# Kernel tuning notes

Hardware: AMD Instinct MI355X
Metric: run time of the kernel (lower is better)

The kernel has to match this reference:

```python
import jax, jax.numpy as jnp
import numpy as np

N, DEG, IN_DIM, HID, OUT = 50000, 32, 256, 256, 128

def setup_inputs() -> dict:
    key = jax.random.key(0)
    k1, k2, k3, k4, k5, k6 = jax.random.split(key, 6)
    node_features = jax.random.normal(k1, (N, IN_DIM), dtype=jnp.float32)
    neighbor_idx = jax.random.randint(k2, (N, DEG), 0, N)
    scale1 = 1.0 / np.sqrt(2 * IN_DIM)
    scale2 = 1.0 / np.sqrt(HID)
    W1 = jax.random.normal(k3, (HID, 2 * IN_DIM), dtype=jnp.float32) * scale1
    b1 = jax.random.normal(k4, (HID,), dtype=jnp.float32) * scale1
    W2 = jax.random.normal(k5, (OUT, HID), dtype=jnp.float32) * scale2
    b2 = jax.random.normal(k6, (OUT,), dtype=jnp.float32) * scale2
    return {"node_features": node_features, "neighbor_idx": neighbor_idx,
            "W1": W1, "b1": b1, "W2": W2, "b2": b2}

def reference(node_features, neighbor_idx, W1, b1, W2, b2):
    # Layer 0 (mean aggregator, with neighbors):
    # gather [N, DEG, IN_DIM] neighbor features, mean over DEG
    nbr_mean = jnp.mean(node_features[neighbor_idx], axis=1)  # [N, IN_DIM]
    combined = jnp.concatenate([node_features, nbr_mean], axis=-1)  # [N, 2*IN_DIM]
    h = jax.nn.relu(combined @ W1.T + b1)  # [N, HID]
    # Layer 1: empty neighbor list -> linear_without_neighbors + relu
    out = jax.nn.relu(h @ W2.T + b2)  # [N, OUT]
    return out
```

## Files before the change

### kernel.cpp

```cpp
#include <hip/hip_runtime.h>
#include <stdint.h>

#define N_NODES 50000
#define DEG     32
#define IN_DIM  256
#define K1      512
#define HID     256
#define OUT_DIM 128

#define NCHUNK  4
#define CDIM    64
#define SLICE8  ((size_t)N_NODES * CDIM)
#define GT      16

#define MT     32
#define NTILES ((N_NODES + MT - 1) / MT)
#define GBLK   512
#define CSTR   520
#define HSTR   264

typedef __bf16 bf16x8 __attribute__((ext_vector_type(8)));
typedef float  f32x4  __attribute__((ext_vector_type(4)));
typedef float  f32x2  __attribute__((ext_vector_type(2)));

#define PIN(x) asm volatile("" : "+v"(x))

__device__ __forceinline__ unsigned short f2bf(float f) {
    union { float f; unsigned u; } v; v.f = f;
    unsigned r = v.u + 0x7fffu + ((v.u >> 16) & 1u);
    return (unsigned short)(r >> 16);
}
__device__ __forceinline__ int clampN(int v) {
    return v < 0 ? 0 : (v >= N_NODES ? N_NODES - 1 : v);
}
__device__ __forceinline__ void async_copy16(const void* g, void* l) {
    __builtin_amdgcn_global_load_lds(
        (const __attribute__((address_space(1))) void*)g,
        (__attribute__((address_space(3))) void*)l, 16, 0, 0);
}

#define FEAT_BLKS ((N_NODES + 7) / 8)
__global__ __launch_bounds__(256)
void prep_all(const float* __restrict__ feat,
              const float* __restrict__ W1, const float* __restrict__ W2,
              const int*   __restrict__ nbr,
              unsigned short* __restrict__ featb,
              unsigned char*  __restrict__ featF8,
              unsigned short* __restrict__ W1b, unsigned short* __restrict__ W2b,
              unsigned short* __restrict__ nbr16)
{
    const int t = threadIdx.x;
    if (blockIdx.x < FEAT_BLKS) {
        const int node = blockIdx.x * 8 + (t >> 5);
        const int seg  = t & 31;
        if (node < N_NODES) {
            const float4* src = (const float4*)(feat + (size_t)node * IN_DIM + seg * 8);
            float4 f0 = src[0], f1 = src[1];
            ushort4 o0, o1;
            o0.x = f2bf(f0.x); o0.y = f2bf(f0.y); o0.z = f2bf(f0.z); o0.w = f2bf(f0.w);
            o1.x = f2bf(f1.x); o1.y = f2bf(f1.y); o1.z = f2bf(f1.z); o1.w = f2bf(f1.w);
            unsigned short* db = featb + (size_t)node * IN_DIM + seg * 8;
            *(ushort4*)db       = o0;
            *(ushort4*)(db + 4) = o1;
            int u0 = 0, u1 = 0;
            u0 = __builtin_amdgcn_cvt_pk_fp8_f32(f0.x, f0.y, u0, false);
            u0 = __builtin_amdgcn_cvt_pk_fp8_f32(f0.z, f0.w, u0, true);
            u1 = __builtin_amdgcn_cvt_pk_fp8_f32(f1.x, f1.y, u1, false);
            u1 = __builtin_amdgcn_cvt_pk_fp8_f32(f1.z, f1.w, u1, true);
            const int c   = seg >> 3;
            const int off = (seg & 7) * 8;
            unsigned char* d8 = featF8 + (size_t)c * SLICE8 + (size_t)node * CDIM + off;
            ((int*)d8)[0] = u0;
            ((int*)d8)[1] = u1;
        }
    } else {
        const int bid = blockIdx.x - FEAT_BLKS;
        const int stride = 256 * 256 * 4;
        const int tid4 = (bid * 256 + t) * 4;
        for (int i = tid4; i < HID * K1; i += stride) {
            float4 f = *(const float4*)(W1 + i);
            ushort4 o; o.x = f2bf(f.x); o.y = f2bf(f.y); o.z = f2bf(f.z); o.w = f2bf(f.w);
            *(ushort4*)(W1b + i) = o;
        }
        for (int i = tid4; i < OUT_DIM * HID; i += stride) {
            float4 f = *(const float4*)(W2 + i);
            ushort4 o; o.x = f2bf(f.x); o.y = f2bf(f.y); o.z = f2bf(f.z); o.w = f2bf(f.w);
            *(ushort4*)(W2b + i) = o;
        }
        for (int i = tid4; i < N_NODES * DEG; i += stride) {
            int4 v = *(const int4*)(nbr + i);
            ushort4 o;
            o.x = (unsigned short)clampN(v.x); o.y = (unsigned short)clampN(v.y);
            o.z = (unsigned short)clampN(v.z); o.w = (unsigned short)clampN(v.w);
            *(ushort4*)(nbr16 + i) = o;
        }
    }
}

__global__ __launch_bounds__(256)
void gather_mean_fp8(const unsigned char*  __restrict__ featF8,
                     const unsigned short* __restrict__ nbr16,
                     unsigned short*       __restrict__ meanb)
{
    __shared__ unsigned short sIdx[GT * DEG];
    const int tid  = threadIdx.x;
    const int c    = blockIdx.y;
    const int base = blockIdx.x * GT;

    if (tid < 128) {
        *(ushort4*)(sIdx + tid * 4) =
            *(const ushort4*)(nbr16 + (size_t)base * DEG + tid * 4);
    }
    __syncthreads();

    const unsigned char* slice = featF8 + (size_t)c * SLICE8;
    const int grp = tid >> 4;
    const int ln  = tid & 15;
    const unsigned short* idxr = sIdx + grp * DEG;

    unsigned vv[DEG];
    #pragma unroll
    for (int j = 0; j < DEG; ++j) {
        int nb = idxr[j];
        vv[j] = *(const unsigned*)(slice + (size_t)nb * CDIM + ln * 4);
    }
    float s0 = 0.f, s1 = 0.f, s2 = 0.f, s3 = 0.f;
    #pragma unroll
    for (int j = 0; j < DEG; ++j) {
        f32x2 lo = __builtin_amdgcn_cvt_pk_f32_fp8(vv[j], false);
        f32x2 hi = __builtin_amdgcn_cvt_pk_f32_fp8(vv[j], true);
        s0 += lo[0]; s1 += lo[1]; s2 += hi[0]; s3 += hi[1];
    }
    const float sc = 1.0f / 32.0f;
    ushort4 o;
    o.x = f2bf(s0 * sc); o.y = f2bf(s1 * sc);
    o.z = f2bf(s2 * sc); o.w = f2bf(s3 * sc);
    const int node = base + grp;
    *(ushort4*)(meanb + (size_t)node * IN_DIM + c * CDIM + ln * 4) = o;
}

__global__ __launch_bounds__(512, 2)
void sage_gemm(const unsigned short* __restrict__ featb,
               const unsigned short* __restrict__ meanb,
               const unsigned short* __restrict__ W1b,
               const float*          __restrict__ b1,
               const unsigned short* __restrict__ W2b,
               const float*          __restrict__ b2,
               float*                __restrict__ out)
{
    __shared__ __align__(16) unsigned short sC[MT * CSTR];
    __shared__ __align__(16) unsigned short sH[MT * HSTR];

    const int tid  = threadIdx.x;
    const int lane = tid & 63;
    const int wave = tid >> 6;
    const int r    = lane & 15;
    const int q    = lane >> 4;

    bf16x8 w1f[2][16];
    #pragma unroll
    for (int nt = 0; nt < 2; ++nt) {
        const size_t nrow = (size_t)(wave * 32 + nt * 16 + r) * K1;
        #pragma unroll
        for (int kk = 0; kk < 16; ++kk) {
            w1f[nt][kk] = *(const bf16x8*)(W1b + nrow + kk * 32 + q * 8);
            PIN(w1f[nt][kk]);
        }
    }
    bf16x8 w2f[8];
    {
        const size_t orow = (size_t)(wave * 16 + r) * HID;
        #pragma unroll
        for (int kk = 0; kk < 8; ++kk) {
            w2f[kk] = *(const bf16x8*)(W2b + orow + kk * 32 + q * 8);
            PIN(w2f[kk]);
        }
    }
    const float bias1a = b1[wave * 32 + r];
    const float bias1b = b1[wave * 32 + 16 + r];
    const float bias2  = b2[wave * 16 + r];

    auto stage = [&](int tile) {
        const int base = tile * MT;
        #pragma unroll
        for (int j = 0; j < 4; ++j) {
            const int i = wave * 4 + j;
            int node = base + i;
            if (node >= N_NODES) node = N_NODES - 1;
            const unsigned short* g = (lane < 32)
                ? featb + (size_t)node * IN_DIM + lane * 8
                : meanb + (size_t)node * IN_DIM + (lane - 32) * 8;
            async_copy16(g, &sC[i * CSTR]);
        }
    };

    int tile = blockIdx.x;
    if (tile < NTILES) stage(tile);

    for (; tile < NTILES; tile += GBLK) {
        __syncthreads();

        {
            f32x4 acc[2][2];
            #pragma unroll
            for (int mt = 0; mt < 2; ++mt)
                #pragma unroll
                for (int nt = 0; nt < 2; ++nt)
                    acc[mt][nt] = (f32x4){0.f, 0.f, 0.f, 0.f};

            #pragma unroll
            for (int kk = 0; kk < 16; ++kk) {
                bf16x8 a0 = *(const bf16x8*)(&sC[r * CSTR + kk * 32 + q * 8]);
                bf16x8 a1 = *(const bf16x8*)(&sC[(16 + r) * CSTR + kk * 32 + q * 8]);
                acc[0][0] = __builtin_amdgcn_mfma_f32_16x16x32_bf16(a0, w1f[0][kk], acc[0][0], 0, 0, 0);
                acc[1][0] = __builtin_amdgcn_mfma_f32_16x16x32_bf16(a1, w1f[0][kk], acc[1][0], 0, 0, 0);
                acc[0][1] = __builtin_amdgcn_mfma_f32_16x16x32_bf16(a0, w1f[1][kk], acc[0][1], 0, 0, 0);
                acc[1][1] = __builtin_amdgcn_mfma_f32_16x16x32_bf16(a1, w1f[1][kk], acc[1][1], 0, 0, 0);
            }
            #pragma unroll
            for (int nt = 0; nt < 2; ++nt) {
                const int n = wave * 32 + nt * 16 + r;
                const float bias = nt ? bias1b : bias1a;
                #pragma unroll
                for (int mt = 0; mt < 2; ++mt)
                    #pragma unroll
                    for (int g = 0; g < 4; ++g) {
                        const int m = mt * 16 + q * 4 + g;
                        float v = acc[mt][nt][g] + bias;
                        sH[m * HSTR + n] = f2bf(v > 0.f ? v : 0.f);
                    }
            }
        }
        __syncthreads();

        const int nxt = tile + GBLK;
        if (nxt < NTILES) stage(nxt);

        {
            f32x4 acc3[2];
            acc3[0] = (f32x4){0.f, 0.f, 0.f, 0.f};
            acc3[1] = (f32x4){0.f, 0.f, 0.f, 0.f};
            #pragma unroll
            for (int kk = 0; kk < 8; ++kk) {
                bf16x8 h0 = *(const bf16x8*)(&sH[r * HSTR + kk * 32 + q * 8]);
                bf16x8 h1 = *(const bf16x8*)(&sH[(16 + r) * HSTR + kk * 32 + q * 8]);
                acc3[0] = __builtin_amdgcn_mfma_f32_16x16x32_bf16(h0, w2f[kk], acc3[0], 0, 0, 0);
                acc3[1] = __builtin_amdgcn_mfma_f32_16x16x32_bf16(h1, w2f[kk], acc3[1], 0, 0, 0);
            }
            const int base = tile * MT;
            const int o = wave * 16 + r;
            #pragma unroll
            for (int mt = 0; mt < 2; ++mt)
                #pragma unroll
                for (int g = 0; g < 4; ++g) {
                    const int m = mt * 16 + q * 4 + g;
                    const int node = base + m;
                    if (node < N_NODES) {
                        float v = acc3[mt][g] + bias2;
                        out[(size_t)node * OUT_DIM + o] = v > 0.f ? v : 0.f;
                    }
                }
        }
    }
}

__global__ __launch_bounds__(256)
void sage_naive(const float* __restrict__ feat, const int* __restrict__ nbr,
                const float* __restrict__ W1, const float* __restrict__ b1,
                const float* __restrict__ W2, const float* __restrict__ b2,
                float* __restrict__ out) {
    __shared__ float comb[K1];
    __shared__ float h[HID];
    const int node = blockIdx.x;
    const int t = threadIdx.x;
    comb[t] = feat[(size_t)node * IN_DIM + t];
    float acc = 0.f;
    for (int d = 0; d < DEG; ++d) {
        int nb = clampN(nbr[node * DEG + d]);
        acc += feat[(size_t)nb * IN_DIM + t];
    }
    comb[IN_DIM + t] = acc * (1.0f / 32.0f);
    __syncthreads();
    float s = b1[t];
    for (int k = 0; k < K1; ++k) s += comb[k] * W1[(size_t)t * K1 + k];
    h[t] = s > 0.f ? s : 0.f;
    __syncthreads();
    if (t < OUT_DIM) {
        float s2 = b2[t];
        for (int k = 0; k < HID; ++k) s2 += h[k] * W2[(size_t)t * HID + k];
        out[(size_t)node * OUT_DIM + t] = s2 > 0.f ? s2 : 0.f;
    }
}

extern "C" void kernel_launch(void* const* d_in, const int* in_sizes, int n_in,
                              void* d_out, int out_size, void* d_ws, size_t ws_size,
                              hipStream_t stream) {
    const float* feat = (const float*)d_in[0];
    const int*   nbr  = (const int*)d_in[1];
    const float* W1   = (const float*)d_in[2];
    const float* b1   = (const float*)d_in[3];
    const float* W2   = (const float*)d_in[4];
    const float* b2   = (const float*)d_in[5];
    float* out = (float*)d_out;

    const size_t feat_elems = (size_t)N_NODES * IN_DIM;
    const size_t w1_elems   = (size_t)HID * K1;
    const size_t w2_elems   = (size_t)OUT_DIM * HID;
    const size_t mean_elems = (size_t)N_NODES * IN_DIM;
    const size_t idx_elems  = (size_t)N_NODES * DEG;
    const size_t u16_elems  = feat_elems + w1_elems + w2_elems + mean_elems + idx_elems;
    const size_t need = u16_elems * sizeof(unsigned short)
                      + (size_t)NCHUNK * SLICE8;

    if (ws_size >= need) {
        unsigned short* featb  = (unsigned short*)d_ws;
        unsigned short* W1b    = featb + feat_elems;
        unsigned short* W2b    = W1b + w1_elems;
        unsigned short* meanb  = W2b + w2_elems;
        unsigned short* nbr16  = meanb + mean_elems;
        unsigned char*  featF8 = (unsigned char*)(nbr16 + idx_elems);

        prep_all<<<FEAT_BLKS + 256, 256, 0, stream>>>(feat, W1, W2, nbr,
                                                      featb, featF8, W1b, W2b, nbr16);
        gather_mean_fp8<<<dim3(N_NODES / GT, NCHUNK), 256, 0, stream>>>(featF8, nbr16, meanb);
        sage_gemm<<<GBLK, 512, 0, stream>>>(featb, meanb, W1b, b1, W2b, b2, out);
    } else {
        sage_naive<<<N_NODES, 256, 0, stream>>>(feat, nbr, W1, b1, W2, b2, out);
    }
}
```

Baseline: 181.2 us.

## Replace persistent register-resident-weight GEMM with LDS-staged K-chunked tiled GEMM

```diff
diff --git a/kernel.cpp b/kernel.cpp
--- a/kernel.cpp
+++ b/kernel.cpp
@@ -13,17 +13,14 @@
 #define SLICE8  ((size_t)N_NODES * CDIM)
 #define GT      16
 
-#define MT     32
-#define NTILES ((N_NODES + MT - 1) / MT)
-#define GBLK   512
-#define CSTR   520
-#define HSTR   264
+#define MT2    64
+#define NT2B   ((N_NODES + MT2 - 1) / MT2)
+#define KC     64
+#define HSTR2  264
 
 typedef __bf16 bf16x8 __attribute__((ext_vector_type(8)));
 typedef float  f32x4  __attribute__((ext_vector_type(4)));
 typedef float  f32x2  __attribute__((ext_vector_type(2)));
-
-#define PIN(x) asm volatile("" : "+v"(x))
 
 __device__ __forceinline__ unsigned short f2bf(float f) {
     union { float f; unsigned u; } v; v.f = f;
@@ -140,127 +137,142 @@
 }
 
 __global__ __launch_bounds__(512, 2)
-void sage_gemm(const unsigned short* __restrict__ featb,
-               const unsigned short* __restrict__ meanb,
-               const unsigned short* __restrict__ W1b,
-               const float*          __restrict__ b1,
-               const unsigned short* __restrict__ W2b,
-               const float*          __restrict__ b2,
-               float*                __restrict__ out)
+void sage_gemm2(const unsigned short* __restrict__ featb,
+                const unsigned short* __restrict__ meanb,
+                const unsigned short* __restrict__ W1b,
+                const float*          __restrict__ b1,
+                const unsigned short* __restrict__ W2b,
+                const float*          __restrict__ b2,
+                float*                __restrict__ out)
 {
-    __shared__ __align__(16) unsigned short sC[MT * CSTR];
-    __shared__ __align__(16) unsigned short sH[MT * HSTR];
+    __shared__ __align__(16) unsigned short sA[MT2 * KC];
+    __shared__ __align__(16) unsigned short sW[256 * KC];
+    __shared__ __align__(16) unsigned short sH[MT2 * HSTR2];
 
     const int tid  = threadIdx.x;
     const int lane = tid & 63;
     const int wave = tid >> 6;
     const int r    = lane & 15;
     const int q    = lane >> 4;
-
-    bf16x8 w1f[2][16];
-    #pragma unroll
-    for (int nt = 0; nt < 2; ++nt) {
-        const size_t nrow = (size_t)(wave * 32 + nt * 16 + r) * K1;
-        #pragma unroll
-        for (int kk = 0; kk < 16; ++kk) {
-            w1f[nt][kk] = *(const bf16x8*)(W1b + nrow + kk * 32 + q * 8);
-            PIN(w1f[nt][kk]);
-        }
-    }
-    bf16x8 w2f[8];
-    {
-        const size_t orow = (size_t)(wave * 16 + r) * HID;
-        #pragma unroll
-        for (int kk = 0; kk < 8; ++kk) {
-            w2f[kk] = *(const bf16x8*)(W2b + orow + kk * 32 + q * 8);
-            PIN(w2f[kk]);
-        }
-    }
-    const float bias1a = b1[wave * 32 + r];
-    const float bias1b = b1[wave * 32 + 16 + r];
-    const float bias2  = b2[wave * 16 + r];
-
-    auto stage = [&](int tile) {
-        const int base = tile * MT;
+    const int mh   = wave >> 2;
+    const int nq   = wave & 3;
+
+    const int tbase = blockIdx.x * MT2;
+
+    f32x4 acc1[2][4];
+    #pragma unroll
+    for (int mt = 0; mt < 2; ++mt)
+        #pragma unroll
+        for (int nt = 0; nt < 4; ++nt)
+            acc1[mt][nt] = (f32x4){0.f, 0.f, 0.f, 0.f};
+
+    for (int kc = 0; kc < 8; ++kc) {
+        __syncthreads();
+        {
+            const int i = wave * 8 + (lane >> 3);
+            const int node = clampN(tbase + i);
+            const int g = (lane & 7) ^ (i & 7);
+            const unsigned short* src = (kc < 4 ? featb : meanb)
+                + (size_t)node * IN_DIM + (kc & 3) * KC + g * 8;
+            async_copy16(src, &sA[wave * 8 * KC]);
+        }
         #pragma unroll
         for (int j = 0; j < 4; ++j) {
-            const int i = wave * 4 + j;
-            int node = base + i;
-            if (node >= N_NODES) node = N_NODES - 1;
-            const unsigned short* g = (lane < 32)
-                ? featb + (size_t)node * IN_DIM + lane * 8
-                : meanb + (size_t)node * IN_DIM + (lane - 32) * 8;
-            async_copy16(g, &sC[i * CSTR]);
-        }
-    };
-
-    int tile = blockIdx.x;
-    if (tile < NTILES) stage(tile);
-
-    for (; tile < NTILES; tile += GBLK) {
+            const int n = wave * 32 + j * 8 + (lane >> 3);
+            const int g = (lane & 7) ^ (n & 7);
+            async_copy16(W1b + (size_t)n * K1 + kc * KC + g * 8,
+                         &sW[(wave * 32 + j * 8) * KC]);
+        }
         __syncthreads();
 
-        {
-            f32x4 acc[2][2];
+        #pragma unroll
+        for (int kk = 0; kk < 2; ++kk) {
+            bf16x8 a[2], w[4];
+            #pragma unroll
+            for (int mt = 0; mt < 2; ++mt)
+                a[mt] = *(const bf16x8*)(&sA[(mh * 32 + mt * 16 + r) * KC
+                                             + ((kk * 4 + q) ^ (r & 7)) * 8]);
+            #pragma unroll
+            for (int nt = 0; nt < 4; ++nt)
+                w[nt] = *(const bf16x8*)(&sW[(nq * 64 + nt * 16 + r) * KC
+                                             + ((kk * 4 + q) ^ (r & 7)) * 8]);
+            #pragma unroll
+            for (int mt = 0; mt < 2; ++mt)
+                #pragma unroll
+                for (int nt = 0; nt < 4; ++nt)
+                    acc1[mt][nt] = __builtin_amdgcn_mfma_f32_16x16x32_bf16(
+                        a[mt], w[nt], acc1[mt][nt], 0, 0, 0);
+        }
+    }
+
+    #pragma unroll
+    for (int nt = 0; nt < 4; ++nt) {
+        const int n = nq * 64 + nt * 16 + r;
+        const float bias = b1[n];
+        #pragma unroll
+        for (int mt = 0; mt < 2; ++mt)
+            #pragma unroll
+            for (int g = 0; g < 4; ++g) {
+                const int m = mh * 32 + mt * 16 + q * 4 + g;
+                float v = acc1[mt][nt][g] + bias;
+                sH[m * HSTR2 + n] = f2bf(v > 0.f ? v : 0.f);
+            }
+    }
+
+    const int nh = wave & 3;
+    f32x4 acc2[2][2];
+    #pragma unroll
+    for (int mt = 0; mt < 2; ++mt)
+        #pragma unroll
+        for (int nt = 0; nt < 2; ++nt)
+            acc2[mt][nt] = (f32x4){0.f, 0.f, 0.f, 0.f};
+
+    for (int kc = 0; kc < 4; ++kc) {
+        __syncthreads();
+        #pragma unroll
+        for (int j = 0; j < 2; ++j) {
+            const int n = wave * 16 + j * 8 + (lane >> 3);
+            const int g = (lane & 7) ^ (n & 7);
+            async_copy16(W2b + (size_t)n * HID + kc * KC + g * 8,
+                         &sW[(wave * 16 + j * 8) * KC]);
+        }
+        __syncthreads();
+
+        #pragma unroll
+        for (int kk = 0; kk < 2; ++kk) {
+            bf16x8 h[2], w[2];
+            #pragma unroll
+            for (int mt = 0; mt < 2; ++mt)
+                h[mt] = *(const bf16x8*)(&sH[(mh * 32 + mt * 16 + r) * HSTR2
+                                             + kc * KC + kk * 32 + q * 8]);
+            #pragma unroll
+            for (int nt = 0; nt < 2; ++nt)
+                w[nt] = *(const bf16x8*)(&sW[(nh * 32 + nt * 16 + r) * KC
+                                             + ((kk * 4 + q) ^ (r & 7)) * 8]);
             #pragma unroll
             for (int mt = 0; mt < 2; ++mt)
                 #pragma unroll
                 for (int nt = 0; nt < 2; ++nt)
-                    acc[mt][nt] = (f32x4){0.f, 0.f, 0.f, 0.f};
-
-            #pragma unroll
-            for (int kk = 0; kk < 16; ++kk) {
-                bf16x8 a0 = *(const bf16x8*)(&sC[r * CSTR + kk * 32 + q * 8]);
-                bf16x8 a1 = *(const bf16x8*)(&sC[(16 + r) * CSTR + kk * 32 + q * 8]);
-                acc[0][0] = __builtin_amdgcn_mfma_f32_16x16x32_bf16(a0, w1f[0][kk], acc[0][0], 0, 0, 0);
-                acc[1][0] = __builtin_amdgcn_mfma_f32_16x16x32_bf16(a1, w1f[0][kk], acc[1][0], 0, 0, 0);
-                acc[0][1] = __builtin_amdgcn_mfma_f32_16x16x32_bf16(a0, w1f[1][kk], acc[0][1], 0, 0, 0);
-                acc[1][1] = __builtin_amdgcn_mfma_f32_16x16x32_bf16(a1, w1f[1][kk], acc[1][1], 0, 0, 0);
+                    acc2[mt][nt] = __builtin_amdgcn_mfma_f32_16x16x32_bf16(
+                        h[mt], w[nt], acc2[mt][nt], 0, 0, 0);
+        }
+    }
+
+    #pragma unroll
+    for (int nt = 0; nt < 2; ++nt) {
+        const int o = nh * 32 + nt * 16 + r;
+        const float bias = b2[o];
+        #pragma unroll
+        for (int mt = 0; mt < 2; ++mt)
+            #pragma unroll
+            for (int g = 0; g < 4; ++g) {
+                const int m = mh * 32 + mt * 16 + q * 4 + g;
+                const int node = tbase + m;
+                if (node < N_NODES) {
+                    float v = acc2[mt][nt][g] + bias;
+                    out[(size_t)node * OUT_DIM + o] = v > 0.f ? v : 0.f;
+                }
             }
-            #pragma unroll
-            for (int nt = 0; nt < 2; ++nt) {
-                const int n = wave * 32 + nt * 16 + r;
-                const float bias = nt ? bias1b : bias1a;
-                #pragma unroll
-                for (int mt = 0; mt < 2; ++mt)
-                    #pragma unroll
-                    for (int g = 0; g < 4; ++g) {
-                        const int m = mt * 16 + q * 4 + g;
-                        float v = acc[mt][nt][g] + bias;
-                        sH[m * HSTR + n] = f2bf(v > 0.f ? v : 0.f);
-                    }
-            }
-        }
-        __syncthreads();
-
-        const int nxt = tile + GBLK;
-        if (nxt < NTILES) stage(nxt);
-
-        {
-            f32x4 acc3[2];
-            acc3[0] = (f32x4){0.f, 0.f, 0.f, 0.f};
-            acc3[1] = (f32x4){0.f, 0.f, 0.f, 0.f};
-            #pragma unroll
-            for (int kk = 0; kk < 8; ++kk) {
-                bf16x8 h0 = *(const bf16x8*)(&sH[r * HSTR + kk * 32 + q * 8]);
-                bf16x8 h1 = *(const bf16x8*)(&sH[(16 + r) * HSTR + kk * 32 + q * 8]);
-                acc3[0] = __builtin_amdgcn_mfma_f32_16x16x32_bf16(h0, w2f[kk], acc3[0], 0, 0, 0);
-                acc3[1] = __builtin_amdgcn_mfma_f32_16x16x32_bf16(h1, w2f[kk], acc3[1], 0, 0, 0);
-            }
-            const int base = tile * MT;
-            const int o = wave * 16 + r;
-            #pragma unroll
-            for (int mt = 0; mt < 2; ++mt)
-                #pragma unroll
-                for (int g = 0; g < 4; ++g) {
-                    const int m = mt * 16 + q * 4 + g;
-                    const int node = base + m;
-                    if (node < N_NODES) {
-                        float v = acc3[mt][g] + bias2;
-                        out[(size_t)node * OUT_DIM + o] = v > 0.f ? v : 0.f;
-                    }
-                }
-        }
     }
 }
 
@@ -323,7 +335,7 @@
         prep_all<<<FEAT_BLKS + 256, 256, 0, stream>>>(feat, W1, W2, nbr,
                                                       featb, featF8, W1b, W2b, nbr16);
         gather_mean_fp8<<<dim3(N_NODES / GT, NCHUNK), 256, 0, stream>>>(featF8, nbr16, meanb);
-        sage_gemm<<<GBLK, 512, 0, stream>>>(featb, meanb, W1b, b1, W2b, b2, out);
+        sage_gemm2<<<NT2B, 512, 0, stream>>>(featb, meanb, W1b, b1, W2b, b2, out);
     } else {
         sage_naive<<<N_NODES, 256, 0, stream>>>(feat, nbr, W1, b1, W2, b2, out);
     }
```

Result: faster. 177.1 us (-2.3%).
